# Kernel tuning notes

Hardware: AMD Instinct MI355X
Metric: run time of the kernel (lower is better)

The kernel has to match this reference:

```python
import jax, jax.numpy as jnp
import numpy as np

GROUPS = 8
NEG_SLOPE = 0.1
EPS = 1e-5


def group_norm(x, gamma, beta):
    # x: (B, N, C). Matches torch GroupNorm applied on (B, C, N):
    # normalize over (channels-in-group, N) per batch per group.
    B, N, C = x.shape
    xg = x.reshape(B, N, GROUPS, C // GROUPS)
    mean = xg.mean(axis=(1, 3), keepdims=True)
    var = xg.var(axis=(1, 3), keepdims=True)
    xg = (xg - mean) * jax.lax.rsqrt(var + EPS)
    return xg.reshape(B, N, C) * gamma + beta


def unary_block(x, W, b, gamma, beta):
    # Linear -> GroupNorm -> LeakyReLU(0.1)
    h = jnp.einsum('bnc,cd->bnd', x, W) + b
    h = group_norm(h, gamma, beta)
    return jnp.where(h >= 0, h, NEG_SLOPE * h)


def setup_inputs() -> dict:
    key = jax.random.key(0)
    ks = jax.random.split(key, 16)
    B, N, M, K, Cin, Cout = 4, 8192, 32768, 16, 128, 128
    inp = {
        'q_feats': jax.random.normal(ks[0], (B, N, Cin), jnp.float32),
        's_feats': jax.random.normal(ks[1], (B, M, Cin), jnp.float32),
        'q_points': jax.random.normal(ks[2], (B, N, 3), jnp.float32),
        's_points': jax.random.normal(ks[3], (B, N, K, 3), jnp.float32),
        'downsample_indices': jax.random.randint(ks[4], (B, N, K), 0, M, jnp.int32),
    }
    sc1 = 1.0 / np.sqrt(Cin)
    sc2 = 1.0 / np.sqrt(Cout)
    inp['W1'] = jax.random.uniform(ks[5], (Cin, Cout), jnp.float32, -sc1, sc1)
    inp['b1'] = jnp.zeros((Cout,), jnp.float32)
    inp['g1'] = jnp.ones((Cout,), jnp.float32)
    inp['be1'] = jnp.zeros((Cout,), jnp.float32)
    inp['W2'] = jax.random.uniform(ks[6], (Cout, Cout), jnp.float32, -sc2, sc2)
    inp['b2'] = jnp.zeros((Cout,), jnp.float32)
    inp['g2'] = jnp.ones((Cout,), jnp.float32)
    inp['be2'] = jnp.zeros((Cout,), jnp.float32)
    inp['W3'] = jax.random.uniform(ks[7], (Cout, Cout), jnp.float32, -sc2, sc2)
    inp['b3'] = jnp.zeros((Cout,), jnp.float32)
    inp['g3'] = jnp.ones((Cout,), jnp.float32)
    inp['be3'] = jnp.zeros((Cout,), jnp.float32)
    return inp


def reference(q_feats, s_feats, q_points, s_points, downsample_indices,
              W1, b1, g1, be1, W2, b2, g2, be2, W3, b3, g3, be3):
    # knn_gather: (B, N, K, C) gathered from (B, M, C)
    grouped = jax.vmap(lambda f, i: f[i])(s_feats, downsample_indices)
    # inverse-squared-distance weights over K neighbors
    d2 = jnp.sum((s_points - q_points[:, :, None, :]) ** 2, axis=-1)  # (B,N,K)
    w = 1.0 / (d2 + 1e-8)
    w = w / jnp.sum(w, axis=-1, keepdims=True)
    latent = jnp.sum(grouped * w[..., None], axis=2)  # (B,N,C)
    h = unary_block(latent, W1, b1, g1, be1)
    h = unary_block(h, W2, b2, g2, be2)
    return unary_block(h + q_feats, W3, b3, g3, be3)
```

## Files before the change

### kernel.cpp

```cpp
#include <hip/hip_runtime.h>


constexpr int NPB = 8192;
constexpr int BN  = 32768;
constexpr int CH  = 128;
constexpr int KNB = 16;
constexpr int MS  = 32768;
constexpr int NG  = 8;
constexpr int CG  = 16;
constexpr int RPB = 64;
constexpr int NBLK = BN / RPB;
constexpr int BPB  = NPB / RPB;
constexpr int MRPB = 16;
constexpr int MNBLK = BN / MRPB;
constexpr int MBPB  = NPB / MRPB;
constexpr int XS = 152;
constexpr int WS = 152;

typedef short short8 __attribute__((ext_vector_type(8)));
typedef float floatx4 __attribute__((ext_vector_type(4)));

static __device__ __forceinline__ unsigned short f2bs(float f) {
    unsigned int u = __builtin_bit_cast(unsigned int, f);
    unsigned int r = (u + 0x7fffu + ((u >> 16) & 1u)) >> 16;
    return (unsigned short)r;
}
static __device__ __forceinline__ float bs2f(unsigned short s) {
    unsigned int u = ((unsigned int)s) << 16;
    return __builtin_bit_cast(float, u);
}

__global__ __launch_bounds__(256) void k_prep(
    const float* __restrict__ W1, const float* __restrict__ W2,
    const float* __restrict__ W3,
    unsigned short* __restrict__ Wt1, unsigned short* __restrict__ Wf2,
    unsigned short* __restrict__ Wf3)
{
    const int bi = blockIdx.x;
    const int w  = bi >> 6;
    const int i  = bi & 63;
    const int el = i * 256 + threadIdx.x;
    const int n  = el >> 7, k = el & 127;
    const float* W = (w == 0) ? W1 : (w == 1) ? W2 : W3;
    unsigned short v = f2bs(W[k * 128 + n]);
    if (w == 0) {
        Wt1[n * 128 + k] = v;
    } else {
        unsigned short* Wf = (w == 1) ? Wf2 : Wf3;
        int j = n >> 4, lr = n & 15;
        int kt = k >> 5, qd = (k >> 3) & 3, e = k & 7;
        Wf[(((j * 4 + kt) * 64) + (qd * 16 + lr)) * 8 + e] = v;
    }
}

__global__ __launch_bounds__(256) void k_head(
    const float* __restrict__ sf, const float* __restrict__ qp,
    const float* __restrict__ sp, const int* __restrict__ idx,
    const unsigned short* __restrict__ Wt,
    const float* __restrict__ bias,
    unsigned short* __restrict__ hout,
    float* __restrict__ part_out)
{
    const int bi = blockIdx.x;
    const int t  = threadIdx.x;
    const int b  = bi / BPB;

    __shared__ unsigned short Xl[RPB * XS];
    __shared__ unsigned short Wl[CH * WS];
    __shared__ float wv[RPB * KNB];
    __shared__ float winv[RPB];
    __shared__ float pw[4][16];

    #pragma unroll
    for (int i = 0; i < 8; i++) {
        int el = i * 2048 + t * 8;
        short8 w8 = *(const short8*)(Wt + el);
        *(short8*)&Wl[(el >> 7) * WS + (el & 127)] = w8;
    }

    #pragma unroll
    for (int i = 0; i < 4; i++) {
        int p = i * 256 + t;
        int row = p >> 4, k = p & 15;
        size_t rg = (size_t)bi * RPB + row;
        float qx = qp[rg * 3 + 0], qy = qp[rg * 3 + 1], qz = qp[rg * 3 + 2];
        const float* spp = sp + (rg * KNB + k) * 3;
        float dx = spp[0] - qx, dy = spp[1] - qy, dz = spp[2] - qz;
        wv[p] = 1.0f / (dx * dx + dy * dy + dz * dz + 1e-8f);
    }
    __syncthreads();
    if (t < RPB) {
        float s = 0.f;
        #pragma unroll
        for (int k = 0; k < KNB; k++) s += wv[t * KNB + k];
        winv[t] = 1.0f / s;
    }
    __syncthreads();
    {
        const int grp = t >> 5, c4 = (t & 31) * 4;
        for (int rr = 0; rr < 8; rr++) {
            int row = grp * 8 + rr;
            size_t rg = (size_t)bi * RPB + row;
            const int* ip = idx + rg * KNB;
            float ax = 0.f, ay = 0.f, az = 0.f, aw = 0.f;
            #pragma unroll
            for (int k = 0; k < KNB; k++) {
                int j = ip[k];
                const float4 f = *(const float4*)(sf + ((size_t)b * MS + j) * CH + c4);
                float w = wv[row * KNB + k];
                ax += w * f.x; ay += w * f.y; az += w * f.z; aw += w * f.w;
            }
            float wi = winv[row];
            ushort4 pk;
            pk.x = f2bs(ax * wi); pk.y = f2bs(ay * wi);
            pk.z = f2bs(az * wi); pk.w = f2bs(aw * wi);
            *(ushort4*)&Xl[row * XS + c4] = pk;
        }
    }
    __syncthreads();

    const int w  = t >> 6;
    const int l  = t & 63;
    const int lr = l & 15;
    const int qd = l >> 4;
    floatx4 acc[8] = {};
    #pragma unroll
    for (int kt = 0; kt < 4; kt++) {
        short8 a = *(const short8*)&Xl[(w * 16 + lr) * XS + kt * 32 + qd * 8];
        #pragma unroll
        for (int j = 0; j < 8; j++) {
            short8 bf = *(const short8*)&Wl[(j * 16 + lr) * WS + kt * 32 + qd * 8];
            acc[j] = __builtin_amdgcn_mfma_f32_16x16x32_bf16(a, bf, acc[j], 0, 0, 0);
        }
    }

    float vals[8][4];
    #pragma unroll
    for (int j = 0; j < 8; j++) {
        float bj = bias[j * 16 + lr];
        float ss = 0.f, qq = 0.f;
        #pragma unroll
        for (int r = 0; r < 4; r++) {
            float v = acc[j][r] + bj;
            vals[j][r] = v;
            ss += v; qq += v * v;
        }
        #pragma unroll
        for (int off = 32; off; off >>= 1) {
            ss += __shfl_down(ss, off);
            qq += __shfl_down(qq, off);
        }
        if (l == 0) { pw[w][j] = ss; pw[w][8 + j] = qq; }
    }
    #pragma unroll
    for (int j = 0; j < 8; j++)
        #pragma unroll
        for (int r = 0; r < 4; r++)
            Xl[(w * 16 + qd * 4 + r) * XS + j * 16 + lr] = f2bs(vals[j][r]);
    __syncthreads();
    if (t < 16)
        part_out[(size_t)bi * 16 + t] = pw[0][t] + pw[1][t] + pw[2][t] + pw[3][t];
    #pragma unroll
    for (int i = 0; i < 4; i++) {
        int flat = i * 2048 + t * 8;
        int row = flat >> 7, col = flat & 127;
        *(short8*)(hout + (size_t)bi * RPB * CH + flat) =
            *(const short8*)&Xl[row * XS + col];
    }
}

template <int RESID, int PPB>
__global__ __launch_bounds__(256) void k_mid(
    const unsigned short* __restrict__ hin,
    const float* __restrict__ part_in,
    const float* __restrict__ gamma,
    const float* __restrict__ beta,
    const float* __restrict__ qf,
    const unsigned short* __restrict__ Wf,
    const float* __restrict__ bias,
    unsigned short* __restrict__ hout,
    float* __restrict__ part_out)
{
    const int bi = blockIdx.x;
    const int t  = threadIdx.x;
    const int b  = bi / MBPB;

    __shared__ unsigned short Xl[MRPB * XS];
    __shared__ float red[16][17];
    __shared__ float2 stats_s[NG];
    __shared__ float pw[4][4];

    constexpr int R = PPB / 16;
    {
        int j = t & 15, chunk = t >> 4;
        float acc = 0.f;
        #pragma unroll
        for (int i = 0; i < R; i++)
            acc += part_in[(size_t)(b * PPB + chunk * R + i) * 16 + j];
        red[chunk][j] = acc;
    }
    __syncthreads();
    if (t < NG) {
        float s = 0.f, q = 0.f;
        #pragma unroll
        for (int c = 0; c < 16; c++) { s += red[c][t]; q += red[c][t + 8]; }
        const float cnt = (float)(NPB * CG);
        float mean = s / cnt;
        float var  = q / cnt - mean * mean;
        stats_s[t] = make_float2(mean, rsqrtf(var + 1e-5f));
    }
    __syncthreads();

    {
        int flat = t * 8;
        int row = flat >> 7, col = flat & 127;
        size_t gidx = (size_t)bi * (MRPB * CH) + flat;
        short8 hv = *(const short8*)(hin + gidx);
        float2 st = stats_s[col >> 4];
        float4 g0 = *(const float4*)(gamma + col);
        float4 g1 = *(const float4*)(gamma + col + 4);
        float4 b0 = *(const float4*)(beta + col);
        float4 b1 = *(const float4*)(beta + col + 4);
        float gg[8] = {g0.x, g0.y, g0.z, g0.w, g1.x, g1.y, g1.z, g1.w};
        float bb[8] = {b0.x, b0.y, b0.z, b0.w, b1.x, b1.y, b1.z, b1.w};
        float re[8];
        if (RESID) {
            float4 r0 = *(const float4*)(qf + gidx);
            float4 r1 = *(const float4*)(qf + gidx + 4);
            re[0]=r0.x; re[1]=r0.y; re[2]=r0.z; re[3]=r0.w;
            re[4]=r1.x; re[5]=r1.y; re[6]=r1.z; re[7]=r1.w;
        }
        unsigned short ov[8];
        #pragma unroll
        for (int e = 0; e < 8; e++) {
            float v = bs2f((unsigned short)hv[e]);
            float y = (v - st.x) * st.y * gg[e] + bb[e];
            y = (y >= 0.f) ? y : 0.1f * y;
            if (RESID) y += re[e];
            ov[e] = f2bs(y);
        }
        *(short8*)&Xl[row * XS + col] = *(short8*)ov;
    }
    __syncthreads();

    const int w  = t >> 6;
    const int l  = t & 63;
    const int lr = l & 15;
    const int qd = l >> 4;
    floatx4 acc2[2] = {};
    #pragma unroll
    for (int kt = 0; kt < 4; kt++) {
        short8 a = *(const short8*)&Xl[lr * XS + kt * 32 + qd * 8];
        #pragma unroll
        for (int jj = 0; jj < 2; jj++) {
            int j = w * 2 + jj;
            short8 bf = *(const short8*)(Wf + (((j * 4 + kt) * 64) + l) * 8);
            acc2[jj] = __builtin_amdgcn_mfma_f32_16x16x32_bf16(a, bf, acc2[jj], 0, 0, 0);
        }
    }

    float vals[2][4];
    #pragma unroll
    for (int jj = 0; jj < 2; jj++) {
        int j = w * 2 + jj;
        float bj = bias[j * 16 + lr];
        float ss = 0.f, qq = 0.f;
        #pragma unroll
        for (int r = 0; r < 4; r++) {
            float v = acc2[jj][r] + bj;
            vals[jj][r] = v;
            ss += v; qq += v * v;
        }
        #pragma unroll
        for (int off = 32; off; off >>= 1) {
            ss += __shfl_down(ss, off);
            qq += __shfl_down(qq, off);
        }
        if (l == 0) { pw[w][jj] = ss; pw[w][2 + jj] = qq; }
    }
    __syncthreads();

    #pragma unroll
    for (int jj = 0; jj < 2; jj++)
        #pragma unroll
        for (int r = 0; r < 4; r++)
            Xl[(qd * 4 + r) * XS + (w * 2 + jj) * 16 + lr] = f2bs(vals[jj][r]);
    if (t < 8)
        part_out[(size_t)bi * 16 + t] = pw[t >> 1][t & 1];
    else if (t < 16) {
        int g = t - 8;
        part_out[(size_t)bi * 16 + t] = pw[g >> 1][2 + (g & 1)];
    }
    __syncthreads();

    {
        int flat = t * 8;
        int row = flat >> 7, col = flat & 127;
        *(short8*)(hout + (size_t)bi * (MRPB * CH) + flat) =
            *(const short8*)&Xl[row * XS + col];
    }
}

__global__ __launch_bounds__(256) void k_out(
    const unsigned short* __restrict__ hin, const float* __restrict__ part_in,
    const float* __restrict__ gamma, const float* __restrict__ beta,
    float* __restrict__ out)
{
    const int bi = blockIdx.x;
    const int t  = threadIdx.x;
    const int b  = bi / MBPB;
    __shared__ float red[16][17];
    __shared__ float2 stats_s[NG];
    constexpr int PPB = 512;
    constexpr int R = PPB / 16;
    {
        int j = t & 15, chunk = t >> 4;
        float acc = 0.f;
        #pragma unroll
        for (int i = 0; i < R; i++)
            acc += part_in[(size_t)(b * PPB + chunk * R + i) * 16 + j];
        red[chunk][j] = acc;
    }
    __syncthreads();
    if (t < NG) {
        float s = 0.f, q = 0.f;
        #pragma unroll
        for (int c = 0; c < 16; c++) { s += red[c][t]; q += red[c][t + 8]; }
        const float cnt = (float)(NPB * CG);
        float mean = s / cnt;
        float var  = q / cnt - mean * mean;
        stats_s[t] = make_float2(mean, rsqrtf(var + 1e-5f));
    }
    __syncthreads();
    {
        int flat = t * 8;
        int col = flat & 127;
        size_t gidx = (size_t)bi * (MRPB * CH) + flat;
        short8 hv = *(const short8*)(hin + gidx);
        float2 st = stats_s[col >> 4];
        float4 g0 = *(const float4*)(gamma + col);
        float4 g1 = *(const float4*)(gamma + col + 4);
        float4 b0 = *(const float4*)(beta + col);
        float4 b1 = *(const float4*)(beta + col + 4);
        float gg[8] = {g0.x, g0.y, g0.z, g0.w, g1.x, g1.y, g1.z, g1.w};
        float bb[8] = {b0.x, b0.y, b0.z, b0.w, b1.x, b1.y, b1.z, b1.w};
        float o[8];
        #pragma unroll
        for (int e = 0; e < 8; e++) {
            float v = bs2f((unsigned short)hv[e]);
            float y = (v - st.x) * st.y * gg[e] + bb[e];
            o[e] = (y >= 0.f) ? y : 0.1f * y;
        }
        float4 o0 = {o[0], o[1], o[2], o[3]};
        float4 o1 = {o[4], o[5], o[6], o[7]};
        *(float4*)(out + gidx)     = o0;
        *(float4*)(out + gidx + 4) = o1;
    }
}

extern "C" void kernel_launch(void* const* d_in, const int* in_sizes, int n_in,
                              void* d_out, int out_size, void* d_ws, size_t ws_size,
                              hipStream_t stream) {
    const float* qf  = (const float*)d_in[0];
    const float* sf  = (const float*)d_in[1];
    const float* qp  = (const float*)d_in[2];
    const float* sp  = (const float*)d_in[3];
    const int*   idx = (const int*)  d_in[4];
    const float* W1  = (const float*)d_in[5];
    const float* b1  = (const float*)d_in[6];
    const float* g1  = (const float*)d_in[7];
    const float* be1 = (const float*)d_in[8];
    const float* W2  = (const float*)d_in[9];
    const float* b2  = (const float*)d_in[10];
    const float* g2  = (const float*)d_in[11];
    const float* be2 = (const float*)d_in[12];
    const float* W3  = (const float*)d_in[13];
    const float* b3  = (const float*)d_in[14];
    const float* g3  = (const float*)d_in[15];
    const float* be3 = (const float*)d_in[16];

    char* ws = (char*)d_ws;
    unsigned short* Wt1 = (unsigned short*)(ws);
    unsigned short* Wf2 = (unsigned short*)(ws + 32768);
    unsigned short* Wf3 = (unsigned short*)(ws + 65536);
    float* p1 = (float*)(ws + 98304);
    float* p2 = (float*)(ws + 131072);
    float* p3 = (float*)(ws + 262144);
    unsigned short* h1 = (unsigned short*)(ws + 393216);
    unsigned short* h2 = (unsigned short*)(ws + 393216 + 8388608);
    unsigned short* h3 = (unsigned short*)(ws + 393216 + 2 * 8388608);
    float* out = (float*)d_out;

    k_prep<<<192, 256, 0, stream>>>(W1, W2, W3, Wt1, Wf2, Wf3);
    k_head<<<NBLK, 256, 0, stream>>>(sf, qp, sp, idx, Wt1, b1, h1, p1);
    k_mid<0, 128><<<MNBLK, 256, 0, stream>>>(h1, p1, g1, be1, nullptr, Wf2, b2, h2, p2);
    k_mid<1, 512><<<MNBLK, 256, 0, stream>>>(h2, p2, g2, be2, qf, Wf3, b3, h3, p3);
    k_out<<<MNBLK, 256, 0, stream>>>(h3, p3, g3, be3, out);
}
```

Baseline: 195.2 us.

## Read pre-swizzled W1 fragments from global in k_head and remap blocks per XCD

k_prep now writes W1 in the same MFMA-fragment-swizzled layout already used for W2 and W3. k_head reads its B operands straight from global memory instead of staging a padded 38KB copy of W1 in LDS. This removes the per-block weight copy and a large share of shared memory, which should allow more resident blocks per CU. The block index is also permuted so each XCD in round-robin dispatch handles a contiguous range of rows from one batch, aiming for better L2 locality on the gathered s_feats. In exchange, weight loads now go through the cache on every MFMA step rather than coming from LDS.

```diff
diff --git a/kernel.cpp b/kernel.cpp
--- a/kernel.cpp
+++ b/kernel.cpp
@@ -15,7 +15,6 @@
 constexpr int MNBLK = BN / MRPB;
 constexpr int MBPB  = NPB / MRPB;
 constexpr int XS = 152;
-constexpr int WS = 152;
 
 typedef short short8 __attribute__((ext_vector_type(8)));
 typedef float floatx4 __attribute__((ext_vector_type(4)));
@@ -33,7 +32,7 @@
 __global__ __launch_bounds__(256) void k_prep(
     const float* __restrict__ W1, const float* __restrict__ W2,
     const float* __restrict__ W3,
-    unsigned short* __restrict__ Wt1, unsigned short* __restrict__ Wf2,
+    unsigned short* __restrict__ Wf1, unsigned short* __restrict__ Wf2,
     unsigned short* __restrict__ Wf3)
 {
     const int bi = blockIdx.x;
@@ -43,40 +42,30 @@
     const int n  = el >> 7, k = el & 127;
     const float* W = (w == 0) ? W1 : (w == 1) ? W2 : W3;
     unsigned short v = f2bs(W[k * 128 + n]);
-    if (w == 0) {
-        Wt1[n * 128 + k] = v;
-    } else {
-        unsigned short* Wf = (w == 1) ? Wf2 : Wf3;
-        int j = n >> 4, lr = n & 15;
-        int kt = k >> 5, qd = (k >> 3) & 3, e = k & 7;
-        Wf[(((j * 4 + kt) * 64) + (qd * 16 + lr)) * 8 + e] = v;
-    }
+    unsigned short* Wf = (w == 0) ? Wf1 : (w == 1) ? Wf2 : Wf3;
+    int j = n >> 4, lr = n & 15;
+    int kt = k >> 5, qd = (k >> 3) & 3, e = k & 7;
+    Wf[(((j * 4 + kt) * 64) + (qd * 16 + lr)) * 8 + e] = v;
 }
 
 __global__ __launch_bounds__(256) void k_head(
     const float* __restrict__ sf, const float* __restrict__ qp,
     const float* __restrict__ sp, const int* __restrict__ idx,
-    const unsigned short* __restrict__ Wt,
+    const unsigned short* __restrict__ Wf,
     const float* __restrict__ bias,
     unsigned short* __restrict__ hout,
     float* __restrict__ part_out)
 {
-    const int bi = blockIdx.x;
-    const int t  = threadIdx.x;
-    const int b  = bi / BPB;
+    const int rep = blockIdx.x & 7;
+    const int q8  = blockIdx.x >> 3;
+    const int bi  = (rep >> 1) * BPB + (rep & 1) * 64 + q8;
+    const int b   = rep >> 1;
+    const int t   = threadIdx.x;
 
     __shared__ unsigned short Xl[RPB * XS];
-    __shared__ unsigned short Wl[CH * WS];
     __shared__ float wv[RPB * KNB];
     __shared__ float winv[RPB];
     __shared__ float pw[4][16];
-
-    #pragma unroll
-    for (int i = 0; i < 8; i++) {
-        int el = i * 2048 + t * 8;
-        short8 w8 = *(const short8*)(Wt + el);
-        *(short8*)&Wl[(el >> 7) * WS + (el & 127)] = w8;
-    }
 
     #pragma unroll
     for (int i = 0; i < 4; i++) {
@@ -129,7 +118,7 @@
         short8 a = *(const short8*)&Xl[(w * 16 + lr) * XS + kt * 32 + qd * 8];
         #pragma unroll
         for (int j = 0; j < 8; j++) {
-            short8 bf = *(const short8*)&Wl[(j * 16 + lr) * WS + kt * 32 + qd * 8];
+            short8 bf = *(const short8*)(Wf + (((j * 4 + kt) * 64) + l) * 8);
             acc[j] = __builtin_amdgcn_mfma_f32_16x16x32_bf16(a, bf, acc[j], 0, 0, 0);
         }
     }
@@ -380,7 +369,7 @@
     const float* be3 = (const float*)d_in[16];
 
     char* ws = (char*)d_ws;
-    unsigned short* Wt1 = (unsigned short*)(ws);
+    unsigned short* Wf1 = (unsigned short*)(ws);
     unsigned short* Wf2 = (unsigned short*)(ws + 32768);
     unsigned short* Wf3 = (unsigned short*)(ws + 65536);
     float* p1 = (float*)(ws + 98304);
@@ -391,8 +380,8 @@
     unsigned short* h3 = (unsigned short*)(ws + 393216 + 2 * 8388608);
     float* out = (float*)d_out;
 
-    k_prep<<<192, 256, 0, stream>>>(W1, W2, W3, Wt1, Wf2, Wf3);
-    k_head<<<NBLK, 256, 0, stream>>>(sf, qp, sp, idx, Wt1, b1, h1, p1);
+    k_prep<<<192, 256, 0, stream>>>(W1, W2, W3, Wf1, Wf2, Wf3);
+    k_head<<<NBLK, 256, 0, stream>>>(sf, qp, sp, idx, Wf1, b1, h1, p1);
     k_mid<0, 128><<<MNBLK, 256, 0, stream>>>(h1, p1, g1, be1, nullptr, Wf2, b2, h2, p2);
     k_mid<1, 512><<<MNBLK, 256, 0, stream>>>(h2, p2, g2, be2, qf, Wf3, b3, h3, p3);
     k_out<<<MNBLK, 256, 0, stream>>>(h3, p3, g3, be3, out);
```

Result: no change. 193.0 us (-1.1%).
